# Kernel tuning notes

Measured on AMD Instinct MI355X. Metric: run time of the kernel, lower is better.

## Reference

```python
import jax, jax.numpy as jnp
import numpy as np

C = 256
CLS_DIM = 512
GROUPS = C // 4
EPS = 1e-5


def group_norm(x, w, b, groups=GROUPS, eps=EPS):
    # x: [N, C, H, W]
    N, Cc, H, W = x.shape
    xg = x.reshape(N, groups, Cc // groups, H, W)
    mu = xg.mean(axis=(2, 3, 4), keepdims=True)
    var = xg.var(axis=(2, 3, 4), keepdims=True)
    xn = ((xg - mu) * jax.lax.rsqrt(var + eps)).reshape(N, Cc, H, W)
    return xn * w[None, :, None, None] + b[None, :, None, None]


def setup_inputs() -> dict:
    key = jax.random.key(0)
    ks = jax.random.split(key, 12)
    N, H, W = 32, 64, 64
    s = 0.02
    return {
        "X": jax.random.normal(ks[0], (N, C, H, W), jnp.float32),
        "cls": jax.random.normal(ks[1], (N, CLS_DIM), jnp.float32),
        "ln_w": 1.0 + s * jax.random.normal(ks[2], (C,), jnp.float32),
        "ln_b": s * jax.random.normal(ks[3], (C,), jnp.float32),
        "wq": jax.random.normal(ks[4], (C, CLS_DIM), jnp.float32) / np.sqrt(CLS_DIM),
        "bq": s * jax.random.normal(ks[5], (C,), jnp.float32),
        "wk": jax.random.normal(ks[6], (C, CLS_DIM), jnp.float32) / np.sqrt(CLS_DIM),
        "bk": s * jax.random.normal(ks[7], (C,), jnp.float32),
        "conv_w": jax.random.normal(ks[8], (C, C), jnp.float32) / np.sqrt(C),
        "conv_b": s * jax.random.normal(ks[9], (C,), jnp.float32),
        "gn_w": 1.0 + s * jax.random.normal(ks[10], (C,), jnp.float32),
        "gn_b": s * jax.random.normal(ks[11], (C,), jnp.float32),
    }


def reference(X, cls, ln_w, ln_b, wq, bq, wk, bk, conv_w, conv_b, gn_w, gn_b):
    res = X
    Xn = group_norm(X, ln_w, ln_b)
    # NOTE: original code swaps names: K <- Q_emb(cls), Q <- K_emb(cls)
    K = jax.nn.elu(cls @ wq.T + bq) + 1.0              # [N, C]
    Q = (jax.nn.elu(cls @ wk.T + bk) + 1.0) / jnp.sqrt(jnp.float32(C))
    # einsum 'nclw,nco->nolw' with o=1: per-pixel channel contraction with K
    s = jnp.einsum("nchw,nc->nhw", Xn, K)              # [N, H, W]
    # einsum 'nolw,nco->nclw': rank-1 outer product with Q
    X2 = s[:, None, :, :] * Q[:, :, None, None]        # [N, C, H, W]
    # 1x1 conv
    Y = jnp.einsum("nchw,oc->nohw", X2, conv_w) + conv_b[None, :, None, None]
    return group_norm(Y, gn_w, gn_b) + res
```

## Files before the change

kernel.cpp:

```cpp
#include <hip/hip_runtime.h>
#include <math.h>

#define EPSV 1e-5f

typedef float f4v __attribute__((ext_vector_type(4)));

__device__ __forceinline__ float waveReduceSum(float v) {
#pragma unroll
    for (int o = 32; o > 0; o >>= 1) v += __shfl_down(v, o, 64);
    return v;
}

__global__ void k_kq(const float* __restrict__ cls,
                     const float* __restrict__ wq, const float* __restrict__ bq,
                     const float* __restrict__ wk, const float* __restrict__ bk,
                     const float* __restrict__ ln_w,
                     float* __restrict__ Kb, float* __restrict__ Qb,
                     float* __restrict__ Kw) {
    int w = blockIdx.x * 4 + (threadIdx.x >> 6);
    int lane = threadIdx.x & 63;
    int n = w >> 8, c = w & 255;
    const float* cp = cls + (size_t)n * 512;
    const float* qp = wq + (size_t)c * 512;
    const float* kp = wk + (size_t)c * 512;
    float aK = 0.f, aQ = 0.f;
#pragma unroll
    for (int i = 0; i < 8; ++i) {
        int kk = lane + i * 64;
        float cv = cp[kk];
        aK += cv * qp[kk];
        aQ += cv * kp[kk];
    }
    aK = waveReduceSum(aK);
    aQ = waveReduceSum(aQ);
    if (lane == 0) {
        float xk = aK + bq[c];
        float xq = aQ + bk[c];
        float Kv = (xk > 0.f ? xk : expf(xk) - 1.f) + 1.f;
        float Qv = ((xq > 0.f ? xq : expf(xq) - 1.f) + 1.f) * 0.0625f;
        Kb[w] = Kv;
        Qb[w] = Qv;
        Kw[w] = Kv * ln_w[c];
    }
}

__global__ void __launch_bounds__(512) k_pass1(
        const float* __restrict__ X, const float* __restrict__ Kw,
        float* __restrict__ W, float* __restrict__ Sp, float* __restrict__ S2p) {
    int n = blockIdx.x >> 4, tile = blockIdx.x & 15;
    int wv = threadIdx.x >> 6, lane = threadIdx.x & 63;
    __shared__ float kws[256];
    if (threadIdx.x < 256) kws[threadIdx.x] = Kw[n * 256 + threadIdx.x];
    __syncthreads();
    int pix = tile * 256 + lane * 4;
    const float* xb = X + ((size_t)n * 256 << 12) + pix;
#pragma unroll
    for (int go = 0; go < 8; ++go) {
        int g = wv * 8 + go;
        int c0 = g * 4;
        float ax = 0.f, ay = 0.f, az = 0.f, aw = 0.f;
        float s = 0.f, s2 = 0.f;
#pragma unroll
        for (int j = 0; j < 4; ++j) {
            float4 v = *(const float4*)(xb + ((size_t)(c0 + j) << 12));
            float kv = kws[c0 + j];
            ax += kv * v.x; ay += kv * v.y; az += kv * v.z; aw += kv * v.w;
            s  += v.x + v.y + v.z + v.w;
            s2 += v.x * v.x + v.y * v.y + v.z * v.z + v.w * v.w;
        }
        float4 acc = {ax, ay, az, aw};
        *(float4*)(W + ((size_t)(n * 64 + g) << 12) + pix) = acc;
        s = waveReduceSum(s);
        s2 = waveReduceSum(s2);
        if (lane == 0) {
            Sp[blockIdx.x * 64 + g] = s;
            S2p[blockIdx.x * 64 + g] = s2;
        }
    }
}

__global__ void k_s(const float* __restrict__ W,
                    const float* __restrict__ Sp, const float* __restrict__ S2p,
                    const float* __restrict__ Kb, const float* __restrict__ Kw,
                    const float* __restrict__ ln_b,
                    const float* __restrict__ Qb, const float* __restrict__ conv_w,
                    float* __restrict__ sbuf,
                    float* __restrict__ p1, float* __restrict__ p2,
                    float* __restrict__ R) {
    int n = blockIdx.x >> 3, tile = blockIdx.x & 7;
    int t = threadIdx.x;
    __shared__ float ivs[64];
    __shared__ float Bsh;
    __shared__ float q1[4], q2[4];
    __shared__ float qs[256];
    if (t < 64) {
        float S = 0.f, S2 = 0.f;
#pragma unroll
        for (int tl = 0; tl < 16; ++tl) {
            S  += Sp[(n * 16 + tl) * 64 + t];
            S2 += S2p[(n * 16 + tl) * 64 + t];
        }
        float mu = S * (1.f / 16384.f);
        float var = S2 * (1.f / 16384.f) - mu * mu;
        float iv = rsqrtf(var + EPSV);
        ivs[t] = iv;
        float t1 = 0.f, t2 = 0.f;
#pragma unroll
        for (int j = 0; j < 4; ++j) {
            int c = t * 4 + j;
            t1 += Kb[n * 256 + c] * ln_b[c];
            t2 += Kw[n * 256 + c];
        }
        float r = waveReduceSum(t1 - iv * mu * t2);
        if (t == 0) Bsh = r;
    }
    __syncthreads();
    int pix = tile * 512 + t * 2;
    const float* wb = W + ((size_t)n * 64 << 12) + pix;
    float Bn = Bsh;
    float sx = Bn, sy = Bn;
#pragma unroll 16
    for (int g = 0; g < 64; ++g) {
        float2 v = *(const float2*)(wb + ((size_t)g << 12));
        float iv = ivs[g];
        sx += iv * v.x; sy += iv * v.y;
    }
    float2 s2v = {sx, sy};
    *(float2*)(sbuf + n * 4096 + pix) = s2v;
    float r1 = waveReduceSum(sx + sy);
    float r2 = waveReduceSum(sx * sx + sy * sy);
    int lane = t & 63, wid = t >> 6;
    if (lane == 0) { q1[wid] = r1; q2[wid] = r2; }
    __syncthreads();
    if (t == 0) {
        p1[blockIdx.x] = q1[0] + q1[1] + q1[2] + q1[3];
        p2[blockIdx.x] = q2[0] + q2[1] + q2[2] + q2[3];
    }
    if (tile == 0) {
        qs[t] = Qb[n * 256 + t];
        __syncthreads();
        const float4* cw = (const float4*)(conv_w + (size_t)t * 256);
        const float4* q4 = (const float4*)qs;
        float acc = 0.f;
#pragma unroll 8
        for (int k = 0; k < 64; ++k) {
            float4 w4 = cw[k], v4 = q4[k];
            acc += w4.x * v4.x + w4.y * v4.y + w4.z * v4.z + w4.w * v4.w;
        }
        R[n * 256 + t] = acc;
    }
}

__global__ void __launch_bounds__(256) k_final(
        const float* __restrict__ X, const float* __restrict__ sbuf,
        const float* __restrict__ p1, const float* __restrict__ p2,
        const float* __restrict__ R, const float* __restrict__ conv_b,
        const float* __restrict__ gn_w, const float* __restrict__ gn_b,
        float* __restrict__ out) {
    size_t idx4 = (size_t)blockIdx.x * 256 + threadIdx.x;
    size_t e0 = (size_t)blockIdx.x * 1024;
    int n = (int)(e0 >> 20);
    int o = (int)((e0 & 1048575) >> 12);

    float a1 = 0.f, a2 = 0.f;
#pragma unroll
    for (int i = 0; i < 8; ++i) { a1 += p1[n * 8 + i]; a2 += p2[n * 8 + i]; }
    float Ms1 = a1 * (1.f / 4096.f);
    float Ms2 = a2 * (1.f / 4096.f);
    int g4 = o & ~3;
    float mR = 0.f, mR2 = 0.f, mRb = 0.f, mb = 0.f, mb2 = 0.f;
#pragma unroll
    for (int j = 0; j < 4; ++j) {
        float r = R[n * 256 + g4 + j];
        float bb = conv_b[g4 + j];
        mR += r; mR2 += r * r; mRb += r * bb; mb += bb; mb2 += bb * bb;
    }
    mR *= 0.25f; mR2 *= 0.25f; mRb *= 0.25f; mb *= 0.25f; mb2 *= 0.25f;
    float mu = Ms1 * mR + mb;
    float var = Ms2 * mR2 + 2.f * Ms1 * mRb + mb2 - mu * mu;
    float iv = rsqrtf(var + EPSV);
    float gw = gn_w[o];
    float a = R[n * 256 + o] * iv * gw;
    float b = (conv_b[o] - mu) * iv * gw + gn_b[o];

    size_t e = idx4 * 4;
    int pix = (int)(e & 4095);
    float4 x = ((const float4*)X)[idx4];
    float4 s = *(const float4*)(sbuf + n * 4096 + pix);
    f4v r;
    r.x = fmaf(s.x, a, b) + x.x;
    r.y = fmaf(s.y, a, b) + x.y;
    r.z = fmaf(s.z, a, b) + x.z;
    r.w = fmaf(s.w, a, b) + x.w;
    __builtin_nontemporal_store(r, (f4v*)out + idx4);
}

extern "C" void kernel_launch(void* const* d_in, const int* in_sizes, int n_in,
                              void* d_out, int out_size, void* d_ws, size_t ws_size,
                              hipStream_t stream) {
    const float* X      = (const float*)d_in[0];
    const float* cls    = (const float*)d_in[1];
    const float* ln_w   = (const float*)d_in[2];
    const float* ln_b   = (const float*)d_in[3];
    const float* wq     = (const float*)d_in[4];
    const float* bq     = (const float*)d_in[5];
    const float* wk     = (const float*)d_in[6];
    const float* bk     = (const float*)d_in[7];
    const float* conv_w = (const float*)d_in[8];
    const float* conv_b = (const float*)d_in[9];
    const float* gn_w   = (const float*)d_in[10];
    const float* gn_b   = (const float*)d_in[11];

    float* ws = (float*)d_ws;
    float* Kb    = ws;
    float* Qb    = ws + 8192;
    float* Kw    = ws + 16384;
    float* Sp    = ws + 24576;
    float* S2p   = ws + 57344;
    float* p1    = ws + 90112;
    float* p2    = ws + 90368;
    float* R     = ws + 90624;
    float* sbuf  = ws + 131072;
    float* W     = ws + 262144;

    k_kq<<<2048, 256, 0, stream>>>(cls, wq, bq, wk, bk, ln_w, Kb, Qb, Kw);
    k_pass1<<<512, 512, 0, stream>>>(X, Kw, W, Sp, S2p);
    k_s<<<256, 256, 0, stream>>>(W, Sp, S2p, Kb, Kw, ln_b, Qb, conv_w,
                                 sbuf, p1, p2, R);
    k_final<<<32768, 256, 0, stream>>>(X, sbuf, p1, p2, R, conv_b, gn_w, gn_b,
                                       (float*)d_out);
}
```

Measured before the change: 91.96 us.

## Drop the intermediate W buffer and recompute the channel contraction from X

The first pass no longer writes per-group K-weighted partial sums to a workspace buffer; it now only computes group-norm statistics. A new fused kernel folds the per-group inverse std into per-channel weights and contracts all 256 channels of X directly, reducing across waves in shared memory. It also raises parallelism from 256 to 512 blocks. This removes the W write and read-back but adds a second full read of X, and relies on X staying resident in the large last-level cache.

Result: slower. 100.5 us (+9.3%).

```diff
diff --git a/kernel.cpp b/kernel.cpp
--- a/kernel.cpp
+++ b/kernel.cpp
@@ -44,32 +44,24 @@
     }
 }
 
-__global__ void __launch_bounds__(512) k_pass1(
-        const float* __restrict__ X, const float* __restrict__ Kw,
-        float* __restrict__ W, float* __restrict__ Sp, float* __restrict__ S2p) {
+__global__ void __launch_bounds__(512) k_stats(
+        const float* __restrict__ X,
+        float* __restrict__ Sp, float* __restrict__ S2p) {
     int n = blockIdx.x >> 4, tile = blockIdx.x & 15;
     int wv = threadIdx.x >> 6, lane = threadIdx.x & 63;
-    __shared__ float kws[256];
-    if (threadIdx.x < 256) kws[threadIdx.x] = Kw[n * 256 + threadIdx.x];
-    __syncthreads();
     int pix = tile * 256 + lane * 4;
     const float* xb = X + ((size_t)n * 256 << 12) + pix;
 #pragma unroll
     for (int go = 0; go < 8; ++go) {
         int g = wv * 8 + go;
         int c0 = g * 4;
-        float ax = 0.f, ay = 0.f, az = 0.f, aw = 0.f;
         float s = 0.f, s2 = 0.f;
 #pragma unroll
         for (int j = 0; j < 4; ++j) {
             float4 v = *(const float4*)(xb + ((size_t)(c0 + j) << 12));
-            float kv = kws[c0 + j];
-            ax += kv * v.x; ay += kv * v.y; az += kv * v.z; aw += kv * v.w;
             s  += v.x + v.y + v.z + v.w;
             s2 += v.x * v.x + v.y * v.y + v.z * v.z + v.w * v.w;
         }
-        float4 acc = {ax, ay, az, aw};
-        *(float4*)(W + ((size_t)(n * 64 + g) << 12) + pix) = acc;
         s = waveReduceSum(s);
         s2 = waveReduceSum(s2);
         if (lane == 0) {
@@ -79,20 +71,24 @@
     }
 }
 
-__global__ void k_s(const float* __restrict__ W,
-                    const float* __restrict__ Sp, const float* __restrict__ S2p,
-                    const float* __restrict__ Kb, const float* __restrict__ Kw,
-                    const float* __restrict__ ln_b,
-                    const float* __restrict__ Qb, const float* __restrict__ conv_w,
-                    float* __restrict__ sbuf,
-                    float* __restrict__ p1, float* __restrict__ p2,
-                    float* __restrict__ R) {
-    int n = blockIdx.x >> 3, tile = blockIdx.x & 7;
-    int t = threadIdx.x;
+__global__ void __launch_bounds__(512) k_sf(
+        const float* __restrict__ X,
+        const float* __restrict__ Sp, const float* __restrict__ S2p,
+        const float* __restrict__ Kb, const float* __restrict__ Kw,
+        const float* __restrict__ ln_b,
+        const float* __restrict__ Qb, const float* __restrict__ conv_w,
+        float* __restrict__ sbuf,
+        float* __restrict__ p1, float* __restrict__ p2,
+        float* __restrict__ R) {
+    int n = blockIdx.x >> 4, tile = blockIdx.x & 15;
+    int t = threadIdx.x, wv = t >> 6, lane = t & 63;
     __shared__ float ivs[64];
+    __shared__ float aS[256];
+    __shared__ float partS[8][256];
+    __shared__ float qs[256];
+    __shared__ float q1[4], q2[4];
     __shared__ float Bsh;
-    __shared__ float q1[4], q2[4];
-    __shared__ float qs[256];
+
     if (t < 64) {
         float S = 0.f, S2 = 0.f;
 #pragma unroll
@@ -115,39 +111,52 @@
         if (t == 0) Bsh = r;
     }
     __syncthreads();
-    int pix = tile * 512 + t * 2;
-    const float* wb = W + ((size_t)n * 64 << 12) + pix;
-    float Bn = Bsh;
-    float sx = Bn, sy = Bn;
-#pragma unroll 16
-    for (int g = 0; g < 64; ++g) {
-        float2 v = *(const float2*)(wb + ((size_t)g << 12));
-        float iv = ivs[g];
-        sx += iv * v.x; sy += iv * v.y;
-    }
-    float2 s2v = {sx, sy};
-    *(float2*)(sbuf + n * 4096 + pix) = s2v;
-    float r1 = waveReduceSum(sx + sy);
-    float r2 = waveReduceSum(sx * sx + sy * sy);
-    int lane = t & 63, wid = t >> 6;
-    if (lane == 0) { q1[wid] = r1; q2[wid] = r2; }
+    if (t < 256) aS[t] = Kw[n * 256 + t] * ivs[t >> 2];
+    __syncthreads();
+
+    int pix = tile * 256 + lane * 4;
+    const float* xb = X + ((size_t)n * 256 << 12) + pix;
+    float ax = 0.f, ay = 0.f, az = 0.f, aw = 0.f;
+#pragma unroll 8
+    for (int j = 0; j < 32; ++j) {
+        int c = wv * 32 + j;
+        float4 v = *(const float4*)(xb + ((size_t)c << 12));
+        float a = aS[c];
+        ax += a * v.x; ay += a * v.y; az += a * v.z; aw += a * v.w;
+    }
+    float4 part = {ax, ay, az, aw};
+    *(float4*)(&partS[wv][lane * 4]) = part;
+    __syncthreads();
+
+    if (t < 256) {
+        float s = Bsh;
+#pragma unroll
+        for (int w = 0; w < 8; ++w) s += partS[w][t];
+        sbuf[n * 4096 + tile * 256 + t] = s;
+        float r1 = waveReduceSum(s);
+        float r2 = waveReduceSum(s * s);
+        if (lane == 0) { q1[wv] = r1; q2[wv] = r2; }
+    }
     __syncthreads();
     if (t == 0) {
         p1[blockIdx.x] = q1[0] + q1[1] + q1[2] + q1[3];
         p2[blockIdx.x] = q2[0] + q2[1] + q2[2] + q2[3];
     }
+
     if (tile == 0) {
-        qs[t] = Qb[n * 256 + t];
+        if (t < 256) qs[t] = Qb[n * 256 + t];
         __syncthreads();
-        const float4* cw = (const float4*)(conv_w + (size_t)t * 256);
-        const float4* q4 = (const float4*)qs;
-        float acc = 0.f;
+        if (t < 256) {
+            const float4* cw = (const float4*)(conv_w + (size_t)t * 256);
+            const float4* q4 = (const float4*)qs;
+            float acc = 0.f;
 #pragma unroll 8
-        for (int k = 0; k < 64; ++k) {
-            float4 w4 = cw[k], v4 = q4[k];
-            acc += w4.x * v4.x + w4.y * v4.y + w4.z * v4.z + w4.w * v4.w;
-        }
-        R[n * 256 + t] = acc;
+            for (int k = 0; k < 64; ++k) {
+                float4 w4 = cw[k], v4 = q4[k];
+                acc += w4.x * v4.x + w4.y * v4.y + w4.z * v4.z + w4.w * v4.w;
+            }
+            R[n * 256 + t] = acc;
+        }
     }
 }
 
@@ -164,7 +173,7 @@
 
     float a1 = 0.f, a2 = 0.f;
 #pragma unroll
-    for (int i = 0; i < 8; ++i) { a1 += p1[n * 8 + i]; a2 += p2[n * 8 + i]; }
+    for (int i = 0; i < 16; ++i) { a1 += p1[n * 16 + i]; a2 += p2[n * 16 + i]; }
     float Ms1 = a1 * (1.f / 4096.f);
     float Ms2 = a2 * (1.f / 4096.f);
     int g4 = o & ~3;
@@ -218,15 +227,14 @@
     float* Sp    = ws + 24576;
     float* S2p   = ws + 57344;
     float* p1    = ws + 90112;
-    float* p2    = ws + 90368;
-    float* R     = ws + 90624;
+    float* p2    = ws + 90624;
+    float* R     = ws + 91136;
     float* sbuf  = ws + 131072;
-    float* W     = ws + 262144;
 
     k_kq<<<2048, 256, 0, stream>>>(cls, wq, bq, wk, bk, ln_w, Kb, Qb, Kw);
-    k_pass1<<<512, 512, 0, stream>>>(X, Kw, W, Sp, S2p);
-    k_s<<<256, 256, 0, stream>>>(W, Sp, S2p, Kb, Kw, ln_b, Qb, conv_w,
-                                 sbuf, p1, p2, R);
+    k_stats<<<512, 512, 0, stream>>>(X, Sp, S2p);
+    k_sf<<<512, 512, 0, stream>>>(X, Sp, S2p, Kb, Kw, ln_b, Qb, conv_w,
+                                  sbuf, p1, p2, R);
     k_final<<<32768, 256, 0, stream>>>(X, sbuf, p1, p2, R, conv_b, gn_w, gn_b,
                                        (float*)d_out);
 }
```
